# Performance work log

Measured on AMD Instinct MI355X. Metric: run time of the kernel, lower is better.

## Reference

```python
import jax, jax.numpy as jnp
import numpy as np

N, E, D = 40000, 640000, 128
BN_EPS = 1e-5


def setup_inputs() -> dict:
    key = jax.random.key(0)
    ks = jax.random.split(key, 6)
    x = jax.random.normal(ks[0], (N, D), dtype=jnp.float32)
    src = jax.random.randint(ks[1], (E,), 0, N, dtype=jnp.int64)
    dst = jax.random.randint(ks[2], (E,), 0, N, dtype=jnp.int64)
    W1 = jax.random.normal(ks[3], (D, D), dtype=jnp.float32) * (1.0 / np.sqrt(D))
    b1 = jnp.zeros((D,), dtype=jnp.float32)
    gamma = jnp.ones((D,), dtype=jnp.float32)
    beta = jnp.zeros((D,), dtype=jnp.float32)
    W2 = jax.random.normal(ks[4], (D, D), dtype=jnp.float32) * (1.0 / np.sqrt(D))
    b2 = jnp.zeros((D,), dtype=jnp.float32)
    eps = jnp.zeros((1,), dtype=jnp.float32)
    return {"x": x, "src": src, "dst": dst, "W1": W1, "b1": b1,
            "gamma": gamma, "beta": beta, "W2": W2, "b2": b2, "eps": eps}


def reference(x, src, dst, W1, b1, gamma, beta, W2, b2, eps):
    # edge gather + ReLU + scatter-sum aggregation  (copy_u -> relu -> sum)
    m = jax.nn.relu(x[src])                                  # [E, D]
    agg = jax.ops.segment_sum(m, dst, num_segments=N)        # [N, D]
    h = (1.0 + eps[0]) * x + agg                             # eps-scaled residual
    # MLP: Linear -> BatchNorm1d (batch stats) -> ReLU -> Linear
    h = h @ W1.T + b1
    mu = jnp.mean(h, axis=0)
    var = jnp.var(h, axis=0)                                 # biased, as torch BN
    h = (h - mu) * jax.lax.rsqrt(var + BN_EPS) * gamma + beta
    h = jax.nn.relu(h)
    return h @ W2.T + b2
```

## Files before the change

### kernel.cpp

```cpp
#include <hip/hip_runtime.h>

#define NN 40000
#define NE 640000
#define DD 128
#define CAP 64

typedef __attribute__((ext_vector_type(8))) short short8;
typedef __attribute__((ext_vector_type(4))) float floatx4;

__device__ __forceinline__ unsigned short f2bf(float f) {
    union { float f; unsigned u; } v; v.f = f;
    return (unsigned short)((v.u + 0x7fffu + ((v.u >> 16) & 1u)) >> 16);
}
__device__ __forceinline__ float bflo2f(unsigned u) {
    union { unsigned u; float f; } v; v.u = u << 16; return v.f;
}
__device__ __forceinline__ float bfhi2f(unsigned u) {
    union { unsigned u; float f; } v; v.u = u & 0xffff0000u; return v.f;
}


__global__ void k_prep(const float* __restrict__ x, const int* __restrict__ src,
                       const int* __restrict__ dst, const float* __restrict__ W1,
                       const float* __restrict__ W2, unsigned short* __restrict__ xb,
                       unsigned short* __restrict__ W1b, unsigned short* __restrict__ W2b,
                       int* __restrict__ cnt, int* __restrict__ eidx) {
    const int tid = blockIdx.x * 256 + threadIdx.x;
    const int P = gridDim.x * 256;
    if (tid < NE) {
        int d = dst[tid];
        int slot = atomicAdd(&cnt[d], 1);
        if (slot < CAP) eidx[d * CAP + slot] = src[tid];
    }
    const float4* x4 = (const float4*)x;
    for (int i = tid; i < NN * DD / 4; i += P) {
        float4 v = x4[i];
        ushort4 o;
        o.x = f2bf(v.x); o.y = f2bf(v.y); o.z = f2bf(v.z); o.w = f2bf(v.w);
        ((ushort4*)xb)[i] = o;
    }
    if (tid < 8192) {
        const float4* w4 = (tid < 4096) ? (const float4*)W1 : (const float4*)W2;
        unsigned short* wb = (tid < 4096) ? W1b : W2b;
        int i = tid & 4095;
        float4 v = w4[i];
        ushort4 o;
        o.x = f2bf(v.x); o.y = f2bf(v.y); o.z = f2bf(v.z); o.w = f2bf(v.w);
        ((ushort4*)wb)[i] = o;
    }
}

__launch_bounds__(256)
__global__ void k_gather(const unsigned short* __restrict__ xb, const int* __restrict__ eidx,
                         const int* __restrict__ cnt, const float* __restrict__ eps,
                         unsigned short* __restrict__ h) {
    const int n = blockIdx.x * 4 + (threadIdx.x >> 6);
    const int lane = threadIdx.x & 63;
    const unsigned* xw = (const unsigned*)xb;
    const float s = 1.0f + eps[0];
    unsigned xv = xw[n * 64 + lane];
    float ax = bflo2f(xv) * s, ay = bfhi2f(xv) * s;
    int deg = cnt[n];
    deg = (deg > CAP) ? CAP : deg;
    const int* row = eidx + n * CAP;
    int j = 0;
    for (; j + 3 < deg; j += 4) {
        int s0 = row[j], s1 = row[j + 1], s2 = row[j + 2], s3 = row[j + 3];
        unsigned v0 = xw[s0 * 64 + lane];
        unsigned v1 = xw[s1 * 64 + lane];
        unsigned v2 = xw[s2 * 64 + lane];
        unsigned v3 = xw[s3 * 64 + lane];
        ax += (fmaxf(bflo2f(v0), 0.f) + fmaxf(bflo2f(v1), 0.f)) +
              (fmaxf(bflo2f(v2), 0.f) + fmaxf(bflo2f(v3), 0.f));
        ay += (fmaxf(bfhi2f(v0), 0.f) + fmaxf(bfhi2f(v1), 0.f)) +
              (fmaxf(bfhi2f(v2), 0.f) + fmaxf(bfhi2f(v3), 0.f));
    }
    for (; j < deg; ++j) {
        unsigned v = xw[row[j] * 64 + lane];
        ax += fmaxf(bflo2f(v), 0.f);
        ay += fmaxf(bfhi2f(v), 0.f);
    }
    ((unsigned*)h)[n * 64 + lane] = ((unsigned)f2bf(ay) << 16) | (unsigned)f2bf(ax);
}

__launch_bounds__(256)
__global__ void k_gemm1(const unsigned short* __restrict__ h,
                        const unsigned short* __restrict__ W1b,
                        const float* __restrict__ b1,
                        float* __restrict__ h1, float* __restrict__ stats) {
    __shared__ float red[2][4][DD];
    const int t = threadIdx.x;
    const int wv = t >> 6, lane = t & 63, m = lane & 15, q = lane >> 4;
    const int r0 = blockIdx.x * 64 + wv * 16;
    floatx4 acc[8];
    #pragma unroll
    for (int nt = 0; nt < 8; ++nt) acc[nt] = (floatx4){0.f, 0.f, 0.f, 0.f};
    const unsigned short* arow = h + (r0 + m) * DD + q * 8;
    const unsigned short* brow = W1b + m * DD + q * 8;
    #pragma unroll
    for (int kt = 0; kt < 4; ++kt) {
        short8 a = *(const short8*)(arow + kt * 32);
        #pragma unroll
        for (int nt = 0; nt < 8; ++nt) {
            short8 b = *(const short8*)(brow + nt * 16 * DD + kt * 32);
            acc[nt] = __builtin_amdgcn_mfma_f32_16x16x32_bf16(a, b, acc[nt], 0, 0, 0);
        }
    }
    #pragma unroll
    for (int nt = 0; nt < 8; ++nt) {
        float bv = b1[nt * 16 + m];
        float cs = 0.f, cq = 0.f;
        #pragma unroll
        for (int r = 0; r < 4; ++r) {
            float v = acc[nt][r] + bv;
            h1[(r0 + q * 4 + r) * DD + nt * 16 + m] = v;
            cs += v;
            cq = fmaf(v, v, cq);
        }
        cs += __shfl_xor(cs, 16); cs += __shfl_xor(cs, 32);
        cq += __shfl_xor(cq, 16); cq += __shfl_xor(cq, 32);
        if (q == 0) { red[0][wv][nt * 16 + m] = cs; red[1][wv][nt * 16 + m] = cq; }
    }
    __syncthreads();
    {
        int plane = t >> 7, j = t & 127;
        float v = (red[plane][0][j] + red[plane][1][j]) + (red[plane][2][j] + red[plane][3][j]);
        atomicAdd(stats + plane * DD + j, v);
    }
}

__launch_bounds__(256)
__global__ void k_gemm2(float* __restrict__ io, const unsigned short* __restrict__ W2b,
                        const float* __restrict__ b2, const float* __restrict__ stats,
                        const float* __restrict__ gamma, const float* __restrict__ beta) {
    __shared__ float ssc[DD], ssh[DD];
    const int t = threadIdx.x;
    if (t < DD) {
        const float inv_n = 1.0f / (float)NN;
        float mu = stats[t] * inv_n;
        float var = stats[DD + t] * inv_n - mu * mu;
        float sc = rsqrtf(var + 1e-5f) * gamma[t];
        ssc[t] = sc;
        ssh[t] = beta[t] - mu * sc;
    }
    __syncthreads();
    const int wv = t >> 6, lane = t & 63, m = lane & 15, q = lane >> 4;
    const int r0 = blockIdx.x * 64 + wv * 16;
    floatx4 acc[8];
    #pragma unroll
    for (int nt = 0; nt < 8; ++nt) acc[nt] = (floatx4){0.f, 0.f, 0.f, 0.f};
    const float* arow = io + (r0 + m) * DD + q * 8;
    const unsigned short* brow = W2b + m * DD + q * 8;
    #pragma unroll
    for (int kt = 0; kt < 4; ++kt) {
        const float* ap = arow + kt * 32;
        const int k0 = kt * 32 + q * 8;
        float4 v0 = *(const float4*)(ap);
        float4 v1 = *(const float4*)(ap + 4);
        float4 c0 = *(const float4*)(ssc + k0);
        float4 c1 = *(const float4*)(ssc + k0 + 4);
        float4 d0 = *(const float4*)(ssh + k0);
        float4 d1 = *(const float4*)(ssh + k0 + 4);
        short8 a;
        a[0] = (short)f2bf(fmaxf(fmaf(v0.x, c0.x, d0.x), 0.f));
        a[1] = (short)f2bf(fmaxf(fmaf(v0.y, c0.y, d0.y), 0.f));
        a[2] = (short)f2bf(fmaxf(fmaf(v0.z, c0.z, d0.z), 0.f));
        a[3] = (short)f2bf(fmaxf(fmaf(v0.w, c0.w, d0.w), 0.f));
        a[4] = (short)f2bf(fmaxf(fmaf(v1.x, c1.x, d1.x), 0.f));
        a[5] = (short)f2bf(fmaxf(fmaf(v1.y, c1.y, d1.y), 0.f));
        a[6] = (short)f2bf(fmaxf(fmaf(v1.z, c1.z, d1.z), 0.f));
        a[7] = (short)f2bf(fmaxf(fmaf(v1.w, c1.w, d1.w), 0.f));
        #pragma unroll
        for (int nt = 0; nt < 8; ++nt) {
            short8 b = *(const short8*)(brow + nt * 16 * DD + kt * 32);
            acc[nt] = __builtin_amdgcn_mfma_f32_16x16x32_bf16(a, b, acc[nt], 0, 0, 0);
        }
    }
    #pragma unroll
    for (int nt = 0; nt < 8; ++nt) {
        float bv = b2[nt * 16 + m];
        #pragma unroll
        for (int r = 0; r < 4; ++r)
            io[(r0 + q * 4 + r) * DD + nt * 16 + m] = acc[nt][r] + bv;
    }
}

extern "C" void kernel_launch(void* const* d_in, const int* in_sizes, int n_in,
                              void* d_out, int out_size, void* d_ws, size_t ws_size,
                              hipStream_t stream) {
    const float* x     = (const float*)d_in[0];
    const int*   src   = (const int*)d_in[1];
    const int*   dst   = (const int*)d_in[2];
    const float* W1    = (const float*)d_in[3];
    const float* b1    = (const float*)d_in[4];
    const float* gamma = (const float*)d_in[5];
    const float* beta  = (const float*)d_in[6];
    const float* W2    = (const float*)d_in[7];
    const float* b2    = (const float*)d_in[8];
    const float* eps   = (const float*)d_in[9];
    float* out = (float*)d_out;

    unsigned short* xb  = (unsigned short*)d_ws;
    unsigned short* h   = xb + NN * DD;
    unsigned short* W1b = h + NN * DD;
    unsigned short* W2b = W1b + DD * DD;
    float* stats = (float*)(W2b + DD * DD);
    int*   cnt   = (int*)(stats + 256);
    int*   eidx  = cnt + NN;

    hipMemsetAsync(stats, 0, (256 + NN) * sizeof(int), stream);
    hipLaunchKernelGGL(k_prep,   dim3(2560),    dim3(256), 0, stream,
                       x, src, dst, W1, W2, xb, W1b, W2b, cnt, eidx);
    hipLaunchKernelGGL(k_gather, dim3(NN / 4),  dim3(256), 0, stream,
                       xb, eidx, cnt, eps, h);
    hipLaunchKernelGGL(k_gemm1,  dim3(NN / 64), dim3(256), 0, stream,
                       h, W1b, b1, out, stats);
    hipLaunchKernelGGL(k_gemm2,  dim3(NN / 64), dim3(256), 0, stream,
                       out, W2b, b2, stats, gamma, beta);
}
```

Measured before the change: 197.9 us.

## Recompute GEMM1 in fused BN+GEMM2 kernel instead of storing fp32 intermediate

The first GEMM kernel now only computes column statistics and no longer writes the fp32 h1 matrix to global memory. The second kernel recomputes GEMM1 from the bf16 aggregate, applies BN and ReLU, stages the result in LDS, and runs GEMM2 from there. This removes a 20MB write and a 20MB read in exchange for doubling the GEMM1 MFMA work. It also spreads the stats atomics across 8 replicas to reduce contention, and unrolls the gather loop by 8 for more memory-level parallelism.

```diff
diff --git a/kernel.cpp b/kernel.cpp
--- a/kernel.cpp
+++ b/kernel.cpp
@@ -4,6 +4,7 @@
 #define NE 640000
 #define DD 128
 #define CAP 64
+#define NREP 8
 
 typedef __attribute__((ext_vector_type(8))) short short8;
 typedef __attribute__((ext_vector_type(4))) float floatx4;
@@ -64,6 +65,26 @@
     deg = (deg > CAP) ? CAP : deg;
     const int* row = eidx + n * CAP;
     int j = 0;
+    for (; j + 7 < deg; j += 8) {
+        int s0 = row[j],     s1 = row[j + 1], s2 = row[j + 2], s3 = row[j + 3];
+        int s4 = row[j + 4], s5 = row[j + 5], s6 = row[j + 6], s7 = row[j + 7];
+        unsigned v0 = xw[s0 * 64 + lane];
+        unsigned v1 = xw[s1 * 64 + lane];
+        unsigned v2 = xw[s2 * 64 + lane];
+        unsigned v3 = xw[s3 * 64 + lane];
+        unsigned v4 = xw[s4 * 64 + lane];
+        unsigned v5 = xw[s5 * 64 + lane];
+        unsigned v6 = xw[s6 * 64 + lane];
+        unsigned v7 = xw[s7 * 64 + lane];
+        ax += ((fmaxf(bflo2f(v0), 0.f) + fmaxf(bflo2f(v1), 0.f)) +
+               (fmaxf(bflo2f(v2), 0.f) + fmaxf(bflo2f(v3), 0.f))) +
+              ((fmaxf(bflo2f(v4), 0.f) + fmaxf(bflo2f(v5), 0.f)) +
+               (fmaxf(bflo2f(v6), 0.f) + fmaxf(bflo2f(v7), 0.f)));
+        ay += ((fmaxf(bfhi2f(v0), 0.f) + fmaxf(bfhi2f(v1), 0.f)) +
+               (fmaxf(bfhi2f(v2), 0.f) + fmaxf(bfhi2f(v3), 0.f))) +
+              ((fmaxf(bfhi2f(v4), 0.f) + fmaxf(bfhi2f(v5), 0.f)) +
+               (fmaxf(bfhi2f(v6), 0.f) + fmaxf(bfhi2f(v7), 0.f)));
+    }
     for (; j + 3 < deg; j += 4) {
         int s0 = row[j], s1 = row[j + 1], s2 = row[j + 2], s3 = row[j + 3];
         unsigned v0 = xw[s0 * 64 + lane];
@@ -84,10 +105,9 @@
 }
 
 __launch_bounds__(256)
-__global__ void k_gemm1(const unsigned short* __restrict__ h,
-                        const unsigned short* __restrict__ W1b,
-                        const float* __restrict__ b1,
-                        float* __restrict__ h1, float* __restrict__ stats) {
+__global__ void k_gemm1s(const unsigned short* __restrict__ h,
+                         const unsigned short* __restrict__ W1b,
+                         const float* __restrict__ b1, float* __restrict__ stats) {
     __shared__ float red[2][4][DD];
     const int t = threadIdx.x;
     const int wv = t >> 6, lane = t & 63, m = lane & 15, q = lane >> 4;
@@ -113,7 +133,6 @@
         #pragma unroll
         for (int r = 0; r < 4; ++r) {
             float v = acc[nt][r] + bv;
-            h1[(r0 + q * 4 + r) * DD + nt * 16 + m] = v;
             cs += v;
             cq = fmaf(v, v, cq);
         }
@@ -125,20 +144,31 @@
     {
         int plane = t >> 7, j = t & 127;
         float v = (red[plane][0][j] + red[plane][1][j]) + (red[plane][2][j] + red[plane][3][j]);
-        atomicAdd(stats + plane * DD + j, v);
+        atomicAdd(stats + (blockIdx.x & (NREP - 1)) * 256 + plane * DD + j, v);
     }
 }
 
 __launch_bounds__(256)
-__global__ void k_gemm2(float* __restrict__ io, const unsigned short* __restrict__ W2b,
-                        const float* __restrict__ b2, const float* __restrict__ stats,
-                        const float* __restrict__ gamma, const float* __restrict__ beta) {
+__global__ void k_gemm2(const unsigned short* __restrict__ h,
+                        const unsigned short* __restrict__ W1b,
+                        const unsigned short* __restrict__ W2b,
+                        const float* __restrict__ b1, const float* __restrict__ b2,
+                        const float* __restrict__ stats,
+                        const float* __restrict__ gamma, const float* __restrict__ beta,
+                        float* __restrict__ out) {
     __shared__ float ssc[DD], ssh[DD];
+    __shared__ __align__(16) unsigned short a2[64][DD + 8];
     const int t = threadIdx.x;
     if (t < DD) {
+        float s0 = 0.f, s1 = 0.f;
+        #pragma unroll
+        for (int rp = 0; rp < NREP; ++rp) {
+            s0 += stats[rp * 256 + t];
+            s1 += stats[rp * 256 + DD + t];
+        }
         const float inv_n = 1.0f / (float)NN;
-        float mu = stats[t] * inv_n;
-        float var = stats[DD + t] * inv_n - mu * mu;
+        float mu = s0 * inv_n;
+        float var = s1 * inv_n - mu * mu;
         float sc = rsqrtf(var + 1e-5f) * gamma[t];
         ssc[t] = sc;
         ssh[t] = beta[t] - mu * sc;
@@ -149,31 +179,41 @@
     floatx4 acc[8];
     #pragma unroll
     for (int nt = 0; nt < 8; ++nt) acc[nt] = (floatx4){0.f, 0.f, 0.f, 0.f};
-    const float* arow = io + (r0 + m) * DD + q * 8;
-    const unsigned short* brow = W2b + m * DD + q * 8;
+    const unsigned short* arow = h + (r0 + m) * DD + q * 8;
+    const unsigned short* brow1 = W1b + m * DD + q * 8;
     #pragma unroll
     for (int kt = 0; kt < 4; ++kt) {
-        const float* ap = arow + kt * 32;
-        const int k0 = kt * 32 + q * 8;
-        float4 v0 = *(const float4*)(ap);
-        float4 v1 = *(const float4*)(ap + 4);
-        float4 c0 = *(const float4*)(ssc + k0);
-        float4 c1 = *(const float4*)(ssc + k0 + 4);
-        float4 d0 = *(const float4*)(ssh + k0);
-        float4 d1 = *(const float4*)(ssh + k0 + 4);
-        short8 a;
-        a[0] = (short)f2bf(fmaxf(fmaf(v0.x, c0.x, d0.x), 0.f));
-        a[1] = (short)f2bf(fmaxf(fmaf(v0.y, c0.y, d0.y), 0.f));
-        a[2] = (short)f2bf(fmaxf(fmaf(v0.z, c0.z, d0.z), 0.f));
-        a[3] = (short)f2bf(fmaxf(fmaf(v0.w, c0.w, d0.w), 0.f));
-        a[4] = (short)f2bf(fmaxf(fmaf(v1.x, c1.x, d1.x), 0.f));
-        a[5] = (short)f2bf(fmaxf(fmaf(v1.y, c1.y, d1.y), 0.f));
-        a[6] = (short)f2bf(fmaxf(fmaf(v1.z, c1.z, d1.z), 0.f));
-        a[7] = (short)f2bf(fmaxf(fmaf(v1.w, c1.w, d1.w), 0.f));
+        short8 a = *(const short8*)(arow + kt * 32);
         #pragma unroll
         for (int nt = 0; nt < 8; ++nt) {
-            short8 b = *(const short8*)(brow + nt * 16 * DD + kt * 32);
+            short8 b = *(const short8*)(brow1 + nt * 16 * DD + kt * 32);
             acc[nt] = __builtin_amdgcn_mfma_f32_16x16x32_bf16(a, b, acc[nt], 0, 0, 0);
+        }
+    }
+    #pragma unroll
+    for (int nt = 0; nt < 8; ++nt) {
+        const int col = nt * 16 + m;
+        float bv = b1[col];
+        float sc = ssc[col], sh = ssh[col];
+        #pragma unroll
+        for (int r = 0; r < 4; ++r) {
+            float v = fmaxf(fmaf(acc[nt][r] + bv, sc, sh), 0.f);
+            a2[wv * 16 + q * 4 + r][col] = f2bf(v);
+        }
+    }
+    __syncthreads();
+    floatx4 acc2[8];
+    #pragma unroll
+    for (int nt = 0; nt < 8; ++nt) acc2[nt] = (floatx4){0.f, 0.f, 0.f, 0.f};
+    const unsigned short* a2row = &a2[wv * 16 + m][0];
+    const unsigned short* brow2 = W2b + m * DD + q * 8;
+    #pragma unroll
+    for (int kt = 0; kt < 4; ++kt) {
+        short8 a = *(const short8*)(a2row + q * 8 + kt * 32);
+        #pragma unroll
+        for (int nt = 0; nt < 8; ++nt) {
+            short8 b = *(const short8*)(brow2 + nt * 16 * DD + kt * 32);
+            acc2[nt] = __builtin_amdgcn_mfma_f32_16x16x32_bf16(a, b, acc2[nt], 0, 0, 0);
         }
     }
     #pragma unroll
@@ -181,7 +221,7 @@
         float bv = b2[nt * 16 + m];
         #pragma unroll
         for (int r = 0; r < 4; ++r)
-            io[(r0 + q * 4 + r) * DD + nt * 16 + m] = acc[nt][r] + bv;
+            out[(r0 + q * 4 + r) * DD + nt * 16 + m] = acc2[nt][r] + bv;
     }
 }
 
@@ -205,16 +245,16 @@
     unsigned short* W1b = h + NN * DD;
     unsigned short* W2b = W1b + DD * DD;
     float* stats = (float*)(W2b + DD * DD);
-    int*   cnt   = (int*)(stats + 256);
+    int*   cnt   = (int*)(stats + NREP * 256);
     int*   eidx  = cnt + NN;
 
-    hipMemsetAsync(stats, 0, (256 + NN) * sizeof(int), stream);
+    hipMemsetAsync(stats, 0, (NREP * 256 + NN) * sizeof(int), stream);
     hipLaunchKernelGGL(k_prep,   dim3(2560),    dim3(256), 0, stream,
                        x, src, dst, W1, W2, xb, W1b, W2b, cnt, eidx);
     hipLaunchKernelGGL(k_gather, dim3(NN / 4),  dim3(256), 0, stream,
                        xb, eidx, cnt, eps, h);
-    hipLaunchKernelGGL(k_gemm1,  dim3(NN / 64), dim3(256), 0, stream,
-                       h, W1b, b1, out, stats);
+    hipLaunchKernelGGL(k_gemm1s, dim3(NN / 64), dim3(256), 0, stream,
+                       h, W1b, b1, stats);
     hipLaunchKernelGGL(k_gemm2,  dim3(NN / 64), dim3(256), 0, stream,
-                       out, W2b, b2, stats, gamma, beta);
-}
+                       h, W1b, W2b, b1, b2, stats, gamma, beta, out);
+}
```

New measurement: 187.8 us. 5.1% less time.

## Fuse neighbor gather into first GEMM, store hidden as bf16, replicate BN stats

Applied to the files above, without the earlier changes.

Merges the gather/aggregate kernel with the first GEMM so the aggregated rows stay in shared memory instead of round-tripping through global memory. The intermediate after GEMM1 is stored as bf16 rather than fp32, and the edge index list uses 16-bit entries. BN statistic atomics are spread over 8 replicas to reduce contention. The trade-off is a much smaller grid with each wave serially processing 16 nodes, which may reduce latency hiding for the random gathers, plus extra bf16 rounding.

```diff
diff --git a/kernel.cpp b/kernel.cpp
--- a/kernel.cpp
+++ b/kernel.cpp
@@ -4,6 +4,8 @@
 #define NE 640000
 #define DD 128
 #define CAP 64
+#define NREP 8
+#define NBLK 625
 
 typedef __attribute__((ext_vector_type(8))) short short8;
 typedef __attribute__((ext_vector_type(4))) float floatx4;
@@ -24,13 +26,13 @@
                        const int* __restrict__ dst, const float* __restrict__ W1,
                        const float* __restrict__ W2, unsigned short* __restrict__ xb,
                        unsigned short* __restrict__ W1b, unsigned short* __restrict__ W2b,
-                       int* __restrict__ cnt, int* __restrict__ eidx) {
+                       int* __restrict__ cnt, unsigned short* __restrict__ eidx) {
     const int tid = blockIdx.x * 256 + threadIdx.x;
     const int P = gridDim.x * 256;
     if (tid < NE) {
         int d = dst[tid];
         int slot = atomicAdd(&cnt[d], 1);
-        if (slot < CAP) eidx[d * CAP + slot] = src[tid];
+        if (slot < CAP) eidx[d * CAP + slot] = (unsigned short)src[tid];
     }
     const float4* x4 = (const float4*)x;
     for (int i = tid; i < NN * DD / 4; i += P) {
@@ -51,125 +53,203 @@
 }
 
 __launch_bounds__(256)
-__global__ void k_gather(const unsigned short* __restrict__ xb, const int* __restrict__ eidx,
-                         const int* __restrict__ cnt, const float* __restrict__ eps,
-                         unsigned short* __restrict__ h) {
-    const int n = blockIdx.x * 4 + (threadIdx.x >> 6);
-    const int lane = threadIdx.x & 63;
-    const unsigned* xw = (const unsigned*)xb;
-    const float s = 1.0f + eps[0];
-    unsigned xv = xw[n * 64 + lane];
-    float ax = bflo2f(xv) * s, ay = bfhi2f(xv) * s;
-    int deg = cnt[n];
-    deg = (deg > CAP) ? CAP : deg;
-    const int* row = eidx + n * CAP;
-    int j = 0;
-    for (; j + 3 < deg; j += 4) {
-        int s0 = row[j], s1 = row[j + 1], s2 = row[j + 2], s3 = row[j + 3];
-        unsigned v0 = xw[s0 * 64 + lane];
-        unsigned v1 = xw[s1 * 64 + lane];
-        unsigned v2 = xw[s2 * 64 + lane];
-        unsigned v3 = xw[s3 * 64 + lane];
-        ax += (fmaxf(bflo2f(v0), 0.f) + fmaxf(bflo2f(v1), 0.f)) +
-              (fmaxf(bflo2f(v2), 0.f) + fmaxf(bflo2f(v3), 0.f));
-        ay += (fmaxf(bfhi2f(v0), 0.f) + fmaxf(bfhi2f(v1), 0.f)) +
-              (fmaxf(bfhi2f(v2), 0.f) + fmaxf(bfhi2f(v3), 0.f));
-    }
-    for (; j < deg; ++j) {
-        unsigned v = xw[row[j] * 64 + lane];
-        ax += fmaxf(bflo2f(v), 0.f);
-        ay += fmaxf(bfhi2f(v), 0.f);
-    }
-    ((unsigned*)h)[n * 64 + lane] = ((unsigned)f2bf(ay) << 16) | (unsigned)f2bf(ax);
-}
-
-__launch_bounds__(256)
-__global__ void k_gemm1(const unsigned short* __restrict__ h,
-                        const unsigned short* __restrict__ W1b,
-                        const float* __restrict__ b1,
-                        float* __restrict__ h1, float* __restrict__ stats) {
+__global__ void k_gg1(const unsigned short* __restrict__ xb, const unsigned short* __restrict__ eidx,
+                      const int* __restrict__ cnt, const float* __restrict__ eps,
+                      const unsigned short* __restrict__ W1b, const float* __restrict__ b1,
+                      unsigned short* __restrict__ h1b, float* __restrict__ stats) {
+    __shared__ __align__(16) unsigned short hbuf[64][DD + 8];
     __shared__ float red[2][4][DD];
     const int t = threadIdx.x;
+    const int wv = t >> 6, lane = t & 63;
+    const int half = lane >> 5, hl = lane & 31;
+    const float s = 1.0f + eps[0];
+    const uint2* xq = (const uint2*)xb;
+
+    for (int i = 0; i < 16; ++i) {
+        const int nl = wv * 16 + i;
+        const int n = blockIdx.x * 64 + nl;
+        float f0, f1, f2, f3;
+        {
+            uint2 xv = xq[n * 32 + hl];
+            float sm = (half == 0) ? s : 0.f;
+            f0 = bflo2f(xv.x) * sm; f1 = bfhi2f(xv.x) * sm;
+            f2 = bflo2f(xv.y) * sm; f3 = bfhi2f(xv.y) * sm;
+        }
+        int deg = cnt[n];
+        deg = (deg > CAP) ? CAP : deg;
+        const unsigned short* row = eidx + n * CAP;
+        int j = 0;
+        for (; j + 15 < deg; j += 16) {
+            int e0 = row[j + half],      e1 = row[j + 2 + half];
+            int e2 = row[j + 4 + half],  e3 = row[j + 6 + half];
+            int e4 = row[j + 8 + half],  e5 = row[j + 10 + half];
+            int e6 = row[j + 12 + half], e7 = row[j + 14 + half];
+            uint2 v0 = xq[e0 * 32 + hl];
+            uint2 v1 = xq[e1 * 32 + hl];
+            uint2 v2 = xq[e2 * 32 + hl];
+            uint2 v3 = xq[e3 * 32 + hl];
+            uint2 v4 = xq[e4 * 32 + hl];
+            uint2 v5 = xq[e5 * 32 + hl];
+            uint2 v6 = xq[e6 * 32 + hl];
+            uint2 v7 = xq[e7 * 32 + hl];
+            f0 += ((fmaxf(bflo2f(v0.x), 0.f) + fmaxf(bflo2f(v1.x), 0.f)) +
+                   (fmaxf(bflo2f(v2.x), 0.f) + fmaxf(bflo2f(v3.x), 0.f))) +
+                  ((fmaxf(bflo2f(v4.x), 0.f) + fmaxf(bflo2f(v5.x), 0.f)) +
+                   (fmaxf(bflo2f(v6.x), 0.f) + fmaxf(bflo2f(v7.x), 0.f)));
+            f1 += ((fmaxf(bfhi2f(v0.x), 0.f) + fmaxf(bfhi2f(v1.x), 0.f)) +
+                   (fmaxf(bfhi2f(v2.x), 0.f) + fmaxf(bfhi2f(v3.x), 0.f))) +
+                  ((fmaxf(bfhi2f(v4.x), 0.f) + fmaxf(bfhi2f(v5.x), 0.f)) +
+                   (fmaxf(bfhi2f(v6.x), 0.f) + fmaxf(bfhi2f(v7.x), 0.f)));
+            f2 += ((fmaxf(bflo2f(v0.y), 0.f) + fmaxf(bflo2f(v1.y), 0.f)) +
+                   (fmaxf(bflo2f(v2.y), 0.f) + fmaxf(bflo2f(v3.y), 0.f))) +
+                  ((fmaxf(bflo2f(v4.y), 0.f) + fmaxf(bflo2f(v5.y), 0.f)) +
+                   (fmaxf(bflo2f(v6.y), 0.f) + fmaxf(bflo2f(v7.y), 0.f)));
+            f3 += ((fmaxf(bfhi2f(v0.y), 0.f) + fmaxf(bfhi2f(v1.y), 0.f)) +
+                   (fmaxf(bfhi2f(v2.y), 0.f) + fmaxf(bfhi2f(v3.y), 0.f))) +
+                  ((fmaxf(bfhi2f(v4.y), 0.f) + fmaxf(bfhi2f(v5.y), 0.f)) +
+                   (fmaxf(bfhi2f(v6.y), 0.f) + fmaxf(bfhi2f(v7.y), 0.f)));
+        }
+        for (; j + 7 < deg; j += 8) {
+            int e0 = row[j + half],     e1 = row[j + 2 + half];
+            int e2 = row[j + 4 + half], e3 = row[j + 6 + half];
+            uint2 v0 = xq[e0 * 32 + hl];
+            uint2 v1 = xq[e1 * 32 + hl];
+            uint2 v2 = xq[e2 * 32 + hl];
+            uint2 v3 = xq[e3 * 32 + hl];
+            f0 += (fmaxf(bflo2f(v0.x), 0.f) + fmaxf(bflo2f(v1.x), 0.f)) +
+                  (fmaxf(bflo2f(v2.x), 0.f) + fmaxf(bflo2f(v3.x), 0.f));
+            f1 += (fmaxf(bfhi2f(v0.x), 0.f) + fmaxf(bfhi2f(v1.x), 0.f)) +
+                  (fmaxf(bfhi2f(v2.x), 0.f) + fmaxf(bfhi2f(v3.x), 0.f));
+            f2 += (fmaxf(bflo2f(v0.y), 0.f) + fmaxf(bflo2f(v1.y), 0.f)) +
+                  (fmaxf(bflo2f(v2.y), 0.f) + fmaxf(bflo2f(v3.y), 0.f));
+            f3 += (fmaxf(bfhi2f(v0.y), 0.f) + fmaxf(bfhi2f(v1.y), 0.f)) +
+                  (fmaxf(bfhi2f(v2.y), 0.f) + fmaxf(bfhi2f(v3.y), 0.f));
+        }
+        for (; j + 1 < deg; j += 2) {
+            int e = row[j + half];
+            uint2 v = xq[e * 32 + hl];
+            f0 += fmaxf(bflo2f(v.x), 0.f); f1 += fmaxf(bfhi2f(v.x), 0.f);
+            f2 += fmaxf(bflo2f(v.y), 0.f); f3 += fmaxf(bfhi2f(v.y), 0.f);
+        }
+        if (j < deg && half == 0) {
+            int e = row[j];
+            uint2 v = xq[e * 32 + hl];
+            f0 += fmaxf(bflo2f(v.x), 0.f); f1 += fmaxf(bfhi2f(v.x), 0.f);
+            f2 += fmaxf(bflo2f(v.y), 0.f); f3 += fmaxf(bfhi2f(v.y), 0.f);
+        }
+        f0 += __shfl_xor(f0, 32); f1 += __shfl_xor(f1, 32);
+        f2 += __shfl_xor(f2, 32); f3 += __shfl_xor(f3, 32);
+        if (half == 0) {
+            unsigned lo = ((unsigned)f2bf(f1) << 16) | (unsigned)f2bf(f0);
+            unsigned hi = ((unsigned)f2bf(f3) << 16) | (unsigned)f2bf(f2);
+            *(uint2*)&hbuf[nl][hl * 4] = make_uint2(lo, hi);
+        }
+    }
+    __syncthreads();
+
+    const int m = lane & 15, q = lane >> 4;
+    floatx4 acc[8];
+    #pragma unroll
+    for (int nt = 0; nt < 8; ++nt) acc[nt] = (floatx4){0.f, 0.f, 0.f, 0.f};
+    {
+        const unsigned short* brow = W1b + m * DD + q * 8;
+        #pragma unroll
+        for (int kt = 0; kt < 4; ++kt) {
+            short8 a = *(const short8*)&hbuf[wv * 16 + m][q * 8 + kt * 32];
+            #pragma unroll
+            for (int nt = 0; nt < 8; ++nt) {
+                short8 b = *(const short8*)(brow + nt * 16 * DD + kt * 32);
+                acc[nt] = __builtin_amdgcn_mfma_f32_16x16x32_bf16(a, b, acc[nt], 0, 0, 0);
+            }
+        }
+    }
+    #pragma unroll
+    for (int nt = 0; nt < 8; ++nt) {
+        float bv = b1[nt * 16 + m];
+        float cs = 0.f, cq = 0.f;
+        #pragma unroll
+        for (int r = 0; r < 4; ++r) {
+            float v = acc[nt][r] + bv;
+            acc[nt][r] = v;
+            cs += v;
+            cq = fmaf(v, v, cq);
+        }
+        cs += __shfl_xor(cs, 16); cs += __shfl_xor(cs, 32);
+        cq += __shfl_xor(cq, 16); cq += __shfl_xor(cq, 32);
+        if (q == 0) { red[0][wv][nt * 16 + m] = cs; red[1][wv][nt * 16 + m] = cq; }
+    }
+    __syncthreads();
+    {
+        int plane = t >> 7, jj = t & 127;
+        float v = (red[plane][0][jj] + red[plane][1][jj]) + (red[plane][2][jj] + red[plane][3][jj]);
+        atomicAdd(stats + (blockIdx.x & (NREP - 1)) * 256 + plane * DD + jj, v);
+    }
+    #pragma unroll
+    for (int nt = 0; nt < 8; ++nt) {
+        const int col = nt * 16 + m;
+        #pragma unroll
+        for (int r = 0; r < 4; ++r)
+            hbuf[wv * 16 + q * 4 + r][col] = f2bf(acc[nt][r]);
+    }
+    __syncthreads();
+    {
+        uint4* dst4 = (uint4*)h1b + blockIdx.x * 1024;
+        #pragma unroll
+        for (int i = 0; i < 4; ++i) {
+            int c = t + 256 * i;
+            int rr = c >> 4, cc = c & 15;
+            dst4[c] = *(const uint4*)&hbuf[rr][cc * 8];
+        }
+    }
+}
+
+__launch_bounds__(256)
+__global__ void k_gemm2(const unsigned short* __restrict__ h1b,
+                        const unsigned short* __restrict__ W2b,
+                        const float* __restrict__ b2, const float* __restrict__ stats,
+                        const float* __restrict__ gamma, const float* __restrict__ beta,
+                        float* __restrict__ out) {
+    __shared__ float ssc[DD], ssh[DD];
+    const int t = threadIdx.x;
+    if (t < DD) {
+        float s0 = 0.f, s1 = 0.f;
+        #pragma unroll
+        for (int rp = 0; rp < NREP; ++rp) {
+            s0 += stats[rp * 256 + t];
+            s1 += stats[rp * 256 + DD + t];
+        }
+        const float inv_n = 1.0f / (float)NN;
+        float mu = s0 * inv_n;
+        float var = s1 * inv_n - mu * mu;
+        float sc = rsqrtf(var + 1e-5f) * gamma[t];
+        ssc[t] = sc;
+        ssh[t] = beta[t] - mu * sc;
+    }
+    __syncthreads();
     const int wv = t >> 6, lane = t & 63, m = lane & 15, q = lane >> 4;
     const int r0 = blockIdx.x * 64 + wv * 16;
     floatx4 acc[8];
     #pragma unroll
     for (int nt = 0; nt < 8; ++nt) acc[nt] = (floatx4){0.f, 0.f, 0.f, 0.f};
-    const unsigned short* arow = h + (r0 + m) * DD + q * 8;
-    const unsigned short* brow = W1b + m * DD + q * 8;
+    const unsigned short* arow = h1b + (r0 + m) * DD + q * 8;
+    const unsigned short* brow = W2b + m * DD + q * 8;
     #pragma unroll
     for (int kt = 0; kt < 4; ++kt) {
-        short8 a = *(const short8*)(arow + kt * 32);
-        #pragma unroll
-        for (int nt = 0; nt < 8; ++nt) {
-            short8 b = *(const short8*)(brow + nt * 16 * DD + kt * 32);
-            acc[nt] = __builtin_amdgcn_mfma_f32_16x16x32_bf16(a, b, acc[nt], 0, 0, 0);
-        }
-    }
-    #pragma unroll
-    for (int nt = 0; nt < 8; ++nt) {
-        float bv = b1[nt * 16 + m];
-        float cs = 0.f, cq = 0.f;
-        #pragma unroll
-        for (int r = 0; r < 4; ++r) {
-            float v = acc[nt][r] + bv;
-            h1[(r0 + q * 4 + r) * DD + nt * 16 + m] = v;
-            cs += v;
-            cq = fmaf(v, v, cq);
-        }
-        cs += __shfl_xor(cs, 16); cs += __shfl_xor(cs, 32);
-        cq += __shfl_xor(cq, 16); cq += __shfl_xor(cq, 32);
-        if (q == 0) { red[0][wv][nt * 16 + m] = cs; red[1][wv][nt * 16 + m] = cq; }
-    }
-    __syncthreads();
-    {
-        int plane = t >> 7, j = t & 127;
-        float v = (red[plane][0][j] + red[plane][1][j]) + (red[plane][2][j] + red[plane][3][j]);
-        atomicAdd(stats + plane * DD + j, v);
-    }
-}
-
-__launch_bounds__(256)
-__global__ void k_gemm2(float* __restrict__ io, const unsigned short* __restrict__ W2b,
-                        const float* __restrict__ b2, const float* __restrict__ stats,
-                        const float* __restrict__ gamma, const float* __restrict__ beta) {
-    __shared__ float ssc[DD], ssh[DD];
-    const int t = threadIdx.x;
-    if (t < DD) {
-        const float inv_n = 1.0f / (float)NN;
-        float mu = stats[t] * inv_n;
-        float var = stats[DD + t] * inv_n - mu * mu;
-        float sc = rsqrtf(var + 1e-5f) * gamma[t];
-        ssc[t] = sc;
-        ssh[t] = beta[t] - mu * sc;
-    }
-    __syncthreads();
-    const int wv = t >> 6, lane = t & 63, m = lane & 15, q = lane >> 4;
-    const int r0 = blockIdx.x * 64 + wv * 16;
-    floatx4 acc[8];
-    #pragma unroll
-    for (int nt = 0; nt < 8; ++nt) acc[nt] = (floatx4){0.f, 0.f, 0.f, 0.f};
-    const float* arow = io + (r0 + m) * DD + q * 8;
-    const unsigned short* brow = W2b + m * DD + q * 8;
-    #pragma unroll
-    for (int kt = 0; kt < 4; ++kt) {
-        const float* ap = arow + kt * 32;
+        uint4 w = *(const uint4*)(arow + kt * 32);
         const int k0 = kt * 32 + q * 8;
-        float4 v0 = *(const float4*)(ap);
-        float4 v1 = *(const float4*)(ap + 4);
         float4 c0 = *(const float4*)(ssc + k0);
         float4 c1 = *(const float4*)(ssc + k0 + 4);
         float4 d0 = *(const float4*)(ssh + k0);
         float4 d1 = *(const float4*)(ssh + k0 + 4);
         short8 a;
-        a[0] = (short)f2bf(fmaxf(fmaf(v0.x, c0.x, d0.x), 0.f));
-        a[1] = (short)f2bf(fmaxf(fmaf(v0.y, c0.y, d0.y), 0.f));
-        a[2] = (short)f2bf(fmaxf(fmaf(v0.z, c0.z, d0.z), 0.f));
-        a[3] = (short)f2bf(fmaxf(fmaf(v0.w, c0.w, d0.w), 0.f));
-        a[4] = (short)f2bf(fmaxf(fmaf(v1.x, c1.x, d1.x), 0.f));
-        a[5] = (short)f2bf(fmaxf(fmaf(v1.y, c1.y, d1.y), 0.f));
-        a[6] = (short)f2bf(fmaxf(fmaf(v1.z, c1.z, d1.z), 0.f));
-        a[7] = (short)f2bf(fmaxf(fmaf(v1.w, c1.w, d1.w), 0.f));
+        a[0] = (short)f2bf(fmaxf(fmaf(bflo2f(w.x), c0.x, d0.x), 0.f));
+        a[1] = (short)f2bf(fmaxf(fmaf(bfhi2f(w.x), c0.y, d0.y), 0.f));
+        a[2] = (short)f2bf(fmaxf(fmaf(bflo2f(w.y), c0.z, d0.z), 0.f));
+        a[3] = (short)f2bf(fmaxf(fmaf(bfhi2f(w.y), c0.w, d0.w), 0.f));
+        a[4] = (short)f2bf(fmaxf(fmaf(bflo2f(w.z), c1.x, d1.x), 0.f));
+        a[5] = (short)f2bf(fmaxf(fmaf(bfhi2f(w.z), c1.y, d1.y), 0.f));
+        a[6] = (short)f2bf(fmaxf(fmaf(bflo2f(w.w), c1.z, d1.z), 0.f));
+        a[7] = (short)f2bf(fmaxf(fmaf(bfhi2f(w.w), c1.w, d1.w), 0.f));
         #pragma unroll
         for (int nt = 0; nt < 8; ++nt) {
             short8 b = *(const short8*)(brow + nt * 16 * DD + kt * 32);
@@ -181,7 +261,7 @@
         float bv = b2[nt * 16 + m];
         #pragma unroll
         for (int r = 0; r < 4; ++r)
-            io[(r0 + q * 4 + r) * DD + nt * 16 + m] = acc[nt][r] + bv;
+            out[(r0 + q * 4 + r) * DD + nt * 16 + m] = acc[nt][r] + bv;
     }
 }
 
@@ -201,20 +281,18 @@
     float* out = (float*)d_out;
 
     unsigned short* xb  = (unsigned short*)d_ws;
-    unsigned short* h   = xb + NN * DD;
-    unsigned short* W1b = h + NN * DD;
+    unsigned short* h1b = xb + NN * DD;
+    unsigned short* W1b = h1b + NN * DD;
     unsigned short* W2b = W1b + DD * DD;
     float* stats = (float*)(W2b + DD * DD);
-    int*   cnt   = (int*)(stats + 256);
-    int*   eidx  = cnt + NN;
-
-    hipMemsetAsync(stats, 0, (256 + NN) * sizeof(int), stream);
-    hipLaunchKernelGGL(k_prep,   dim3(2560),    dim3(256), 0, stream,
+    int*   cnt   = (int*)(stats + NREP * 256);
+    unsigned short* eidx = (unsigned short*)(cnt + NN);
+
+    hipMemsetAsync(stats, 0, (NREP * 256 + NN) * sizeof(int), stream);
+    hipLaunchKernelGGL(k_prep, dim3(2560), dim3(256), 0, stream,
                        x, src, dst, W1, W2, xb, W1b, W2b, cnt, eidx);
-    hipLaunchKernelGGL(k_gather, dim3(NN / 4),  dim3(256), 0, stream,
-                       xb, eidx, cnt, eps, h);
-    hipLaunchKernelGGL(k_gemm1,  dim3(NN / 64), dim3(256), 0, stream,
-                       h, W1b, b1, out, stats);
-    hipLaunchKernelGGL(k_gemm2,  dim3(NN / 64), dim3(256), 0, stream,
-                       out, W2b, b2, stats, gamma, beta);
-}
+    hipLaunchKernelGGL(k_gg1,  dim3(NBLK), dim3(256), 0, stream,
+                       xb, eidx, cnt, eps, W1b, b1, h1b, stats);
+    hipLaunchKernelGGL(k_gemm2, dim3(NBLK), dim3(256), 0, stream,
+                       h1b, W2b, b2, stats, gamma, beta, out);
+}
```

New measurement: 198.7 us. About the same (+0.4%).
